# Performance work log

Hardware: AMD Instinct MI355X
Metric: run time of the kernel (lower is better)

Reference implementation:

```python
import jax, jax.numpy as jnp
import numpy as np
import math

D_MODEL = 768
H = 12
D_K = D_MODEL // H
KSIZE = 3  # 2*suppression_radius+1


def setup_inputs() -> dict:
    key = jax.random.key(0)
    ks = jax.random.split(key, 12)
    B, S = 8, 1024
    s = 1.0 / math.sqrt(D_MODEL)
    return {
        "q": jax.random.normal(ks[0], (B, S, D_MODEL), jnp.float32),
        "k": jax.random.normal(ks[1], (B, S, D_MODEL), jnp.float32),
        "v": jax.random.normal(ks[2], (B, S, D_MODEL), jnp.float32),
        "wq": jax.random.normal(ks[3], (D_MODEL, D_MODEL), jnp.float32) * s,
        "bq": jnp.zeros((D_MODEL,), jnp.float32),
        "wk": jax.random.normal(ks[4], (D_MODEL, D_MODEL), jnp.float32) * s,
        "bk": jnp.zeros((D_MODEL,), jnp.float32),
        "wv": jax.random.normal(ks[5], (D_MODEL, D_MODEL), jnp.float32) * s,
        "bv": jnp.zeros((D_MODEL,), jnp.float32),
        "wo": jax.random.normal(ks[6], (D_MODEL, D_MODEL), jnp.float32) * s,
        "bo": jnp.zeros((D_MODEL,), jnp.float32),
        "conv_w": jax.random.normal(ks[7], (H, 1, KSIZE, KSIZE), jnp.float32) * 0.1,
    }


def reference(q, k, v, wq, bq, wk, bk, wv, bv, wo, bo, conv_w):
    B, S, _ = q.shape
    # projections -> [B, h, S, d_k]
    Q = (q @ wq.T + bq).reshape(B, S, H, D_K).transpose(0, 2, 1, 3)
    K = (k @ wk.T + bk).reshape(B, S, H, D_K).transpose(0, 2, 1, 3)
    V = (v @ wv.T + bv).reshape(B, S, H, D_K).transpose(0, 2, 1, 3)
    scale = 1.0 / math.sqrt(D_K)
    scores = jnp.einsum("bhqd,bhkd->bhqk", Q, K) * scale  # [B,h,S,S]
    # per-head depthwise 3x3 conv over the score "image" (SAME padding, no bias)
    supp = jax.lax.conv_general_dilated(
        scores, conv_w, window_strides=(1, 1), padding="SAME",
        dimension_numbers=("NCHW", "OIHW", "NCHW"), feature_group_count=H)
    probs = jax.nn.softmax(scores - supp, axis=-1)
    out = jnp.einsum("bhqk,bhkd->bhqd", probs, V)
    out = out.transpose(0, 2, 1, 3).reshape(B, S, D_MODEL)
    return out @ wo.T + bo
```

## Files before the change

### kernel.cpp

```cpp
#include <hip/hip_runtime.h>
#include <math.h>

typedef __attribute__((ext_vector_type(8))) short short8;
typedef __attribute__((ext_vector_type(4))) float f32x4;
typedef __attribute__((ext_vector_type(16))) float f32x16;
typedef __attribute__((ext_vector_type(4))) unsigned short ushort4v;
typedef __attribute__((ext_vector_type(4))) unsigned int u32x4;

#define D_MODEL 768
#define NH      12
#define DK      64
#define SEQ     1024
#define NB      8
#define MTOT    (NB*SEQ)
#define NELT    ((size_t)MTOT*D_MODEL)
#define WELT    ((size_t)D_MODEL*D_MODEL)
#define L2E     1.44269504088896f

__device__ __forceinline__ unsigned short f2bf(float f) {
    unsigned int u = __builtin_bit_cast(unsigned int, f);
    unsigned int r = (u + 0x7FFFu + ((u >> 16) & 1u)) >> 16;
    return (unsigned short)r;
}
__device__ __forceinline__ float bf2f(unsigned short h) {
    return __builtin_bit_cast(float, ((unsigned int)h) << 16);
}
__device__ __forceinline__ float fast_exp2(float x) {
#if __has_builtin(__builtin_amdgcn_exp2f)
    return __builtin_amdgcn_exp2f(x);
#else
    return __expf(x * 0.69314718056f);
#endif
}
__device__ __forceinline__ unsigned int pk_bf16_rn(float lo, float hi) {
    unsigned int ul = __builtin_bit_cast(unsigned int, lo) + 0x8000u;
    unsigned int uh = __builtin_bit_cast(unsigned int, hi) + 0x8000u;
    return __builtin_amdgcn_perm(uh, ul, 0x07060302u);
}
__device__ __forceinline__ void plswap(unsigned int &a, unsigned int &b, int g) {
#if __has_builtin(__builtin_amdgcn_permlane32_swap)
    typedef __attribute__((ext_vector_type(2))) unsigned int uint2v;
    uint2v r = __builtin_amdgcn_permlane32_swap(a, b, false, false);
    a = r[0]; b = r[1];
#else
    unsigned int sa = __shfl_xor(a, 32), sb = __shfl_xor(b, 32);
    unsigned int na = g ? sb : a;
    unsigned int nb = g ? b : sa;
    a = na; b = nb;
#endif
}
__device__ __forceinline__ void gload_lds16(const void* g, void* lds) {
    __builtin_amdgcn_global_load_lds(
        (const __attribute__((address_space(1))) unsigned int*)g,
        (__attribute__((address_space(3))) unsigned int*)lds, 16, 0, 0);
}

__global__ __launch_bounds__(256) void cvt_all(
    const float* __restrict__ q, const float* __restrict__ k, const float* __restrict__ v,
    const float* __restrict__ wq, const float* __restrict__ wk,
    const float* __restrict__ wv, const float* __restrict__ wo,
    unsigned short* __restrict__ qb, unsigned short* __restrict__ kb, unsigned short* __restrict__ vb,
    unsigned short* __restrict__ wqb, unsigned short* __restrict__ wkb,
    unsigned short* __restrict__ wvb, unsigned short* __restrict__ wob)
{
    size_t i = (size_t)blockIdx.x * 256 + threadIdx.x;
    const size_t per = NELT / 8, wper = WELT / 8;
    const float* s; unsigned short* d; size_t l;
    if (i < per)            { s = q;  d = qb;  l = i; }
    else if (i < 2*per)     { s = k;  d = kb;  l = i - per; }
    else if (i < 3*per)     { s = v;  d = vb;  l = i - 2*per; }
    else {
        size_t j = i - 3*per;
        if (j < wper)        { s = wq; d = wqb; l = j; }
        else if (j < 2*wper) { s = wk; d = wkb; l = j - wper; }
        else if (j < 3*wper) { s = wv; d = wvb; l = j - 2*wper; }
        else                 { s = wo; d = wob; l = j - 3*wper; }
    }
    const float4* sp = (const float4*)(s + l*8);
    float4 v0 = sp[0], v1 = sp[1];
    short8 o;
    o[0]=(short)f2bf(v0.x); o[1]=(short)f2bf(v0.y); o[2]=(short)f2bf(v0.z); o[3]=(short)f2bf(v0.w);
    o[4]=(short)f2bf(v1.x); o[5]=(short)f2bf(v1.y); o[6]=(short)f2bf(v1.z); o[7]=(short)f2bf(v1.w);
    *(short8*)(d + l*8) = o;
}

#define BM 128
#define BN 128
#define BKG 64

__global__ __launch_bounds__(256) void proj_gemm(
    const unsigned short* __restrict__ Aq, const unsigned short* __restrict__ Ak,
    const unsigned short* __restrict__ Av,
    const unsigned short* __restrict__ Wq, const unsigned short* __restrict__ Wk,
    const unsigned short* __restrict__ Wv,
    const float* __restrict__ bq, const float* __restrict__ bk, const float* __restrict__ bv,
    unsigned short* __restrict__ Qp, unsigned short* __restrict__ Kp,
    unsigned short* __restrict__ Vtp)
{
    __shared__ unsigned short As[BM*BKG];
    __shared__ unsigned short Bs[BN*BKG];
    const int tid = threadIdx.x;
    const int lane = tid & 63, wid = tid >> 6;
    const int wr = wid >> 1, wc = wid & 1;
    const int m0 = blockIdx.y * BM, n0 = blockIdx.x * BN;
    const int z = blockIdx.z;

    const unsigned short* A = (z == 0) ? Aq : (z == 1) ? Ak : Av;
    const unsigned short* W = (z == 0) ? Wq : (z == 1) ? Wk : Wv;
    const float* bias       = (z == 0) ? bq : (z == 1) ? bk : bv;

    f32x4 acc[4][4];
    #pragma unroll
    for (int i = 0; i < 4; ++i)
        #pragma unroll
        for (int j = 0; j < 4; ++j) acc[i][j] = (f32x4)(0.f);

    for (int k0 = 0; k0 < D_MODEL; k0 += BKG) {
        __syncthreads();
        #pragma unroll
        for (int j = 0; j < 4; ++j) {
            int p = ((wid*4 + j) << 9) + lane*8;
            int row = p >> 6, off = p & 63;
            const unsigned short* srcA = A + (size_t)(m0+row)*D_MODEL + k0 + (off ^ ((row&7)<<3));
            gload_lds16(srcA, &As[(wid*4 + j) << 9]);
            const unsigned short* srcB = W + (size_t)(n0+row)*D_MODEL + k0 + (off ^ ((row&7)<<3));
            gload_lds16(srcB, &Bs[(wid*4 + j) << 9]);
        }
        __syncthreads();
        #pragma unroll
        for (int ks = 0; ks < 2; ++ks) {
            short8 af[4], bf8[4];
            #pragma unroll
            for (int mi = 0; mi < 4; ++mi) {
                int row = wr*64 + mi*16 + (lane & 15);
                af[mi] = *(const short8*)&As[row*BKG + ((ks*32 + (lane>>4)*8) ^ ((row&7)<<3))];
            }
            #pragma unroll
            for (int ni = 0; ni < 4; ++ni) {
                int row = wc*64 + ni*16 + (lane & 15);
                bf8[ni] = *(const short8*)&Bs[row*BKG + ((ks*32 + (lane>>4)*8) ^ ((row&7)<<3))];
            }
            #pragma unroll
            for (int mi = 0; mi < 4; ++mi)
                #pragma unroll
                for (int ni = 0; ni < 4; ++ni)
                    acc[mi][ni] = __builtin_amdgcn_mfma_f32_16x16x32_bf16(af[mi], bf8[ni], acc[mi][ni], 0, 0, 0);
        }
    }

    float bv4[4];
    #pragma unroll
    for (int ni = 0; ni < 4; ++ni) bv4[ni] = bias[n0 + wc*64 + ni*16 + (lane & 15)];

    if (z < 2) {
        unsigned short* C = (z == 0) ? Qp : Kp;
        const float scale = (z == 0) ? 0.125f : 1.0f;
        #pragma unroll
        for (int mi = 0; mi < 4; ++mi)
            #pragma unroll
            for (int ni = 0; ni < 4; ++ni) {
                int col = n0 + wc*64 + ni*16 + (lane & 15);
                int rbase = m0 + wr*64 + mi*16 + ((lane>>4)<<2);
                #pragma unroll
                for (int j = 0; j < 4; ++j)
                    C[(size_t)(rbase+j)*D_MODEL + col] = f2bf((acc[mi][ni][j] + bv4[ni]) * scale);
            }
    } else {
        #pragma unroll
        for (int mi = 0; mi < 4; ++mi)
            #pragma unroll
            for (int ni = 0; ni < 4; ++ni) {
                int col = n0 + wc*64 + ni*16 + (lane & 15);
                int hh = col >> 6, dd = col & 63;
                int m = m0 + wr*64 + mi*16 + ((lane>>4)<<2);
                int bb = m >> 10, ss = m & (SEQ-1);
                ushort4v pk;
                #pragma unroll
                for (int j = 0; j < 4; ++j) pk[j] = f2bf(acc[mi][ni][j] + bv4[ni]);
                *(ushort4v*)&Vtp[((size_t)(bb*NH + hh)*DK + dd)*SEQ + ss] = pk;
            }
    }
}

__global__ __launch_bounds__(256) void gemm_out(
    const unsigned short* __restrict__ A, const unsigned short* __restrict__ W,
    const float* __restrict__ bias, float* __restrict__ C)
{
    __shared__ unsigned short As[BM*BKG];
    __shared__ unsigned short Bs[BN*BKG];
    const int tid = threadIdx.x;
    const int lane = tid & 63, wid = tid >> 6;
    const int wr = wid >> 1, wc = wid & 1;
    const int m0 = blockIdx.y * BM, n0 = blockIdx.x * BN;

    f32x4 acc[4][4];
    #pragma unroll
    for (int i = 0; i < 4; ++i)
        #pragma unroll
        for (int j = 0; j < 4; ++j) acc[i][j] = (f32x4)(0.f);

    for (int k0 = 0; k0 < D_MODEL; k0 += BKG) {
        __syncthreads();
        #pragma unroll
        for (int j = 0; j < 4; ++j) {
            int p = ((wid*4 + j) << 9) + lane*8;
            int row = p >> 6, off = p & 63;
            const unsigned short* srcA = A + (size_t)(m0+row)*D_MODEL + k0 + (off ^ ((row&7)<<3));
            gload_lds16(srcA, &As[(wid*4 + j) << 9]);
            const unsigned short* srcB = W + (size_t)(n0+row)*D_MODEL + k0 + (off ^ ((row&7)<<3));
            gload_lds16(srcB, &Bs[(wid*4 + j) << 9]);
        }
        __syncthreads();
        #pragma unroll
        for (int ks = 0; ks < 2; ++ks) {
            short8 af[4], bf8[4];
            #pragma unroll
            for (int mi = 0; mi < 4; ++mi) {
                int row = wr*64 + mi*16 + (lane & 15);
                af[mi] = *(const short8*)&As[row*BKG + ((ks*32 + (lane>>4)*8) ^ ((row&7)<<3))];
            }
            #pragma unroll
            for (int ni = 0; ni < 4; ++ni) {
                int row = wc*64 + ni*16 + (lane & 15);
                bf8[ni] = *(const short8*)&Bs[row*BKG + ((ks*32 + (lane>>4)*8) ^ ((row&7)<<3))];
            }
            #pragma unroll
            for (int mi = 0; mi < 4; ++mi)
                #pragma unroll
                for (int ni = 0; ni < 4; ++ni)
                    acc[mi][ni] = __builtin_amdgcn_mfma_f32_16x16x32_bf16(af[mi], bf8[ni], acc[mi][ni], 0, 0, 0);
        }
    }

    float bv4[4];
    #pragma unroll
    for (int ni = 0; ni < 4; ++ni) bv4[ni] = bias[n0 + wc*64 + ni*16 + (lane & 15)];

    #pragma unroll
    for (int mi = 0; mi < 4; ++mi)
        #pragma unroll
        for (int ni = 0; ni < 4; ++ni) {
            int col = n0 + wc*64 + ni*16 + (lane & 15);
            int rbase = m0 + wr*64 + mi*16 + ((lane>>4)<<2);
            #pragma unroll
            for (int j = 0; j < 4; ++j)
                C[(size_t)(rbase+j)*D_MODEL + col] = acc[mi][ni][j] + bv4[ni];
        }
}

#define KVB 64
#define NCH (SEQ/KVB)
#define THR 8.0f

__global__ __launch_bounds__(256, 3) void attn_flash(
    const unsigned short* __restrict__ Qp,
    const unsigned short* __restrict__ Kp,
    const unsigned short* __restrict__ Vt,
    const float* __restrict__ CW,
    unsigned short* __restrict__ Aop)
{
    __shared__ unsigned short Ks[2][66*64];
    __shared__ unsigned short Vs[2][64*64];

    const int tid = threadIdx.x;
    const int lane = tid & 63, wid = tid >> 6;
    const int ql = lane & 31, g = lane >> 5;

    const int bid = blockIdx.x;
    const int sw = (bid & 7) * 96 + (bid >> 3);
    const int q0 = (sw & 7) * 128;
    const int bh = sw >> 3;
    const int h = bh % NH, b = bh / NH;

    float wcv[9];
    #pragma unroll
    for (int i = 0; i < 9; ++i) wcv[i] = CW[h*9 + i];

    const unsigned short* KpB = Kp + (size_t)b*SEQ*D_MODEL + h*DK;
    const unsigned short* QpB = Qp + (size_t)b*SEQ*D_MODEL + h*DK;
    const char* VtB = (const char*)Vt + (size_t)bh*DK*SEQ*2;

    short8 kreg[3];
    auto kload = [&](int ck) {
        #pragma unroll
        for (int u = 0; u < 3; ++u) {
            int idx = tid + u*256;
            short8 v = (short8)0;
            if (idx < 528) {
                int r = idx >> 3, oct = idx & 7;
                int gk = ck*KVB - 1 + r;
                if (gk >= 0 && gk < SEQ)
                    v = *(const short8*)&KpB[(size_t)gk*D_MODEL + oct*8];
            }
            kreg[u] = v;
        }
    };
    auto kstore = [&](int buf) {
        #pragma unroll
        for (int u = 0; u < 3; ++u) {
            int idx = tid + u*256;
            if (idx < 528) {
                int r = idx >> 3, oct = idx & 7;
                *(short8*)&Ks[buf][r*64 + ((oct ^ (r&7)) << 3)] = kreg[u];
            }
        }
    };
    auto vstage = [&](int ck, int buf) {
        #pragma unroll
        for (int u = 0; u < 2; ++u) {
            int p = (tid + u*256) * 16;
            int row = p >> 7, off = p & 127;
            const char* src = VtB + ((size_t)row*SEQ + ck*KVB)*2 + (off ^ ((row&7)<<4));
            gload_lds16(src, (char*)Vs[buf] + p);
        }
    };

    kload(0);

    short8 qtf[3][4];
    {
        int gq = q0 + wid*32 + ql;
        #pragma unroll
        for (int i = 0; i < 4; ++i) {
            int dwin = i*16 + g*8;
            short8 qm = (short8)0, qc, qp8 = (short8)0;
            if (gq > 0)      qm  = *(const short8*)&QpB[(size_t)(gq-1)*D_MODEL + dwin];
            qc = *(const short8*)&QpB[(size_t)gq*D_MODEL + dwin];
            if (gq < SEQ-1)  qp8 = *(const short8*)&QpB[(size_t)(gq+1)*D_MODEL + dwin];
            short8 f0, f1, f2;
            #pragma unroll
            for (int j = 0; j < 8; ++j) {
                float fm = bf2f((unsigned short)qm[j]);
                float fc = bf2f((unsigned short)qc[j]);
                float fp = bf2f((unsigned short)qp8[j]);
                float t0 = (fc - (wcv[1]*fm + wcv[4]*fc + wcv[7]*fp)) * L2E;
                float t1 = -(wcv[0]*fm + wcv[3]*fc + wcv[6]*fp) * L2E;
                float t2 = -(wcv[2]*fm + wcv[5]*fc + wcv[8]*fp) * L2E;
                f0[j] = (short)f2bf(t0);
                f1[j] = (short)f2bf(t1);
                f2[j] = (short)f2bf(t2);
            }
            qtf[0][i] = f0; qtf[1][i] = f1; qtf[2][i] = f2;
        }
    }
    kstore(0);
    vstage(0, 0);
    __syncthreads();

    float m = -1e30f, l = 0.f;
    f32x16 oac[2];
    oac[0] = (f32x16)(0.f); oac[1] = (f32x16)(0.f);

    int cur = 0;
    for (int ck = 0; ck < NCH; ++ck) {
        if (ck < NCH-1) { kload(ck+1); vstage(ck+1, cur^1); }

        f32x16 st2[2];
        #pragma unroll
        for (int t = 0; t < 2; ++t) {
            f32x16 s = (f32x16)(0.f);
            #pragma unroll
            for (int sl = 0; sl < 3; ++sl) {
                const int shift = (sl == 0) ? 1 : (sl == 1) ? 0 : 2;
                int ar = t*32 + ql + shift;
                #pragma unroll
                for (int i = 0; i < 4; ++i) {
                    int oct = 2*i + g;
                    short8 a = *(const short8*)&Ks[cur][ar*64 + ((oct ^ (ar&7)) << 3)];
                    s = __builtin_amdgcn_mfma_f32_32x32x16_bf16(a, qtf[sl][i], s, 0, 0, 0);
                }
            }
            st2[t] = s;
        }

        float tmax = -1e30f;
        #pragma unroll
        for (int t = 0; t < 2; ++t)
            #pragma unroll
            for (int j = 0; j < 16; ++j) tmax = fmaxf(tmax, st2[t][j]);
        tmax = fmaxf(tmax, __shfl_xor(tmax, 32));

        if (!__all(tmax - m <= THR)) {
            float mn = fmaxf(m, tmax);
            float r = fast_exp2(m - mn);
            l *= r;
            #pragma unroll
            for (int dt = 0; dt < 2; ++dt)
                #pragma unroll
                for (int j = 0; j < 16; ++j) oac[dt][j] *= r;
            m = mn;
        }
        float lsum = 0.f;
        #pragma unroll
        for (int t = 0; t < 2; ++t)
            #pragma unroll
            for (int j = 0; j < 16; ++j) {
                float e = fast_exp2(st2[t][j] - m);
                st2[t][j] = e;
                lsum += e;
            }
        lsum += __shfl_xor(lsum, 32);
        l += lsum;

        short8 pf[4];
        #pragma unroll
        for (int t = 0; t < 2; ++t) {
            #pragma unroll
            for (int f = 0; f < 2; ++f) {
                const int base = f*8;
                unsigned int x0 = pk_bf16_rn(st2[t][base+0], st2[t][base+1]);
                unsigned int x1 = pk_bf16_rn(st2[t][base+2], st2[t][base+3]);
                unsigned int y0 = pk_bf16_rn(st2[t][base+4], st2[t][base+5]);
                unsigned int y1 = pk_bf16_rn(st2[t][base+6], st2[t][base+7]);
                plswap(x0, y0, g);
                plswap(x1, y1, g);
                u32x4 w = {x0, x1, y0, y1};
                pf[t*2 + f] = __builtin_bit_cast(short8, w);
            }
        }

        #pragma unroll
        for (int f = 0; f < 4; ++f) {
            #pragma unroll
            for (int dt = 0; dt < 2; ++dt) {
                int vr = dt*32 + ql;
                int oct = 2*f + g;
                short8 a = *(const short8*)&Vs[cur][vr*64 + ((oct ^ (vr&7)) << 3)];
                oac[dt] = __builtin_amdgcn_mfma_f32_32x32x16_bf16(a, pf[f], oac[dt], 0, 0, 0);
            }
        }

        if (ck < NCH-1) kstore(cur^1);
        __syncthreads();
        cur ^= 1;
    }

    float invl = 1.0f / l;
    int qg = q0 + wid*32 + ql;
    size_t obase = (size_t)(b*SEQ + qg)*D_MODEL + h*DK;
    #pragma unroll
    for (int dt = 0; dt < 2; ++dt) {
        #pragma unroll
        for (int u = 0; u < 4; ++u) {
            int d0 = dt*32 + 8*u + 4*g;
            ushort4v o;
            #pragma unroll
            for (int j = 0; j < 4; ++j) o[j] = f2bf(oac[dt][4*u + j] * invl);
            *(ushort4v*)&Aop[obase + d0] = o;
        }
    }
}

extern "C" void kernel_launch(void* const* d_in, const int* in_sizes, int n_in,
                              void* d_out, int out_size, void* d_ws, size_t ws_size,
                              hipStream_t stream)
{
    const float* q  = (const float*)d_in[0];
    const float* k  = (const float*)d_in[1];
    const float* v  = (const float*)d_in[2];
    const float* wq = (const float*)d_in[3];
    const float* bq = (const float*)d_in[4];
    const float* wk = (const float*)d_in[5];
    const float* bk = (const float*)d_in[6];
    const float* wv = (const float*)d_in[7];
    const float* bv = (const float*)d_in[8];
    const float* wo = (const float*)d_in[9];
    const float* bo = (const float*)d_in[10];
    const float* cw = (const float*)d_in[11];

    unsigned short* qb  = (unsigned short*)d_ws;
    unsigned short* kb  = qb  + NELT;
    unsigned short* vb  = kb  + NELT;
    unsigned short* wqb = vb  + NELT;
    unsigned short* wkb = wqb + WELT;
    unsigned short* wvb = wkb + WELT;
    unsigned short* wob = wvb + WELT;
    unsigned short* Qp  = wob + WELT;
    unsigned short* Kp  = Qp  + NELT;
    unsigned short* Vtp = Kp  + NELT;
    unsigned short* Aop = Vtp + NELT;

    const int cvtBlocks = (int)((3*NELT + 4*WELT) / 8 / 256);
    cvt_all<<<cvtBlocks, 256, 0, stream>>>(q, k, v, wq, wk, wv, wo,
                                           qb, kb, vb, wqb, wkb, wvb, wob);

    dim3 gg(D_MODEL/BN, MTOT/BM, 3);
    proj_gemm<<<gg, 256, 0, stream>>>(qb, kb, vb, wqb, wkb, wvb, bq, bk, bv, Qp, Kp, Vtp);

    attn_flash<<<dim3(768), 256, 0, stream>>>(Qp, Kp, Vtp, cw, Aop);

    gemm_out<<<dim3(D_MODEL/BN, MTOT/BM), 256, 0, stream>>>(Aop, wob, bo, (float*)d_out);
}
```

Baseline: 165.1 us.

## Fuse activation fp32-to-bf16 conversion into projection GEMM and remap blocks per XCD

Drops the separate pass that converted the q/k/v activations to bf16. The projection GEMM now loads fp32 activation tiles straight into LDS with a swizzled layout and converts them to bf16 when building the MFMA fragments, so one full write and re-read of three bf16 activation tensors goes away. It also flattens the launch grid and maps block ids so each XCD covers a contiguous range of M tiles, aiming for better L2 reuse. In exchange, A tiles take twice the LDS and global-load bandwidth per tile, and every k-step repeats the conversion work across the column warps.

```diff
diff --git a/kernel.cpp b/kernel.cpp
--- a/kernel.cpp
+++ b/kernel.cpp
@@ -1,4 +1,5 @@
 #include <hip/hip_runtime.h>
+#include <hip/hip_bf16.h>
 #include <math.h>
 
 typedef __attribute__((ext_vector_type(8))) short short8;
@@ -21,6 +22,10 @@
     unsigned int u = __builtin_bit_cast(unsigned int, f);
     unsigned int r = (u + 0x7FFFu + ((u >> 16) & 1u)) >> 16;
     return (unsigned short)r;
+}
+__device__ __forceinline__ unsigned short f2bf_rne(float f) {
+    __hip_bfloat16 h = __float2bfloat16(f);
+    return __builtin_bit_cast(unsigned short, h);
 }
 __device__ __forceinline__ float bf2f(unsigned short h) {
     return __builtin_bit_cast(float, ((unsigned int)h) << 16);
@@ -55,27 +60,19 @@
         (__attribute__((address_space(3))) unsigned int*)lds, 16, 0, 0);
 }
 
-__global__ __launch_bounds__(256) void cvt_all(
-    const float* __restrict__ q, const float* __restrict__ k, const float* __restrict__ v,
-    const float* __restrict__ wq, const float* __restrict__ wk,
-    const float* __restrict__ wv, const float* __restrict__ wo,
-    unsigned short* __restrict__ qb, unsigned short* __restrict__ kb, unsigned short* __restrict__ vb,
-    unsigned short* __restrict__ wqb, unsigned short* __restrict__ wkb,
-    unsigned short* __restrict__ wvb, unsigned short* __restrict__ wob)
+__global__ __launch_bounds__(256) void cvt_w(
+    const float* __restrict__ a, const float* __restrict__ b,
+    const float* __restrict__ c, const float* __restrict__ e,
+    unsigned short* __restrict__ oa, unsigned short* __restrict__ ob,
+    unsigned short* __restrict__ oc, unsigned short* __restrict__ oe)
 {
     size_t i = (size_t)blockIdx.x * 256 + threadIdx.x;
-    const size_t per = NELT / 8, wper = WELT / 8;
+    const size_t per = WELT / 8;
     const float* s; unsigned short* d; size_t l;
-    if (i < per)            { s = q;  d = qb;  l = i; }
-    else if (i < 2*per)     { s = k;  d = kb;  l = i - per; }
-    else if (i < 3*per)     { s = v;  d = vb;  l = i - 2*per; }
-    else {
-        size_t j = i - 3*per;
-        if (j < wper)        { s = wq; d = wqb; l = j; }
-        else if (j < 2*wper) { s = wk; d = wkb; l = j - wper; }
-        else if (j < 3*wper) { s = wv; d = wvb; l = j - 2*wper; }
-        else                 { s = wo; d = wob; l = j - 3*wper; }
-    }
+    if (i < per)        { s = a; d = oa; l = i; }
+    else if (i < 2*per) { s = b; d = ob; l = i - per; }
+    else if (i < 3*per) { s = c; d = oc; l = i - 2*per; }
+    else                { s = e; d = oe; l = i - 3*per; }
     const float4* sp = (const float4*)(s + l*8);
     float4 v0 = sp[0], v1 = sp[1];
     short8 o;
@@ -89,23 +86,28 @@
 #define BKG 64
 
 __global__ __launch_bounds__(256) void proj_gemm(
-    const unsigned short* __restrict__ Aq, const unsigned short* __restrict__ Ak,
-    const unsigned short* __restrict__ Av,
+    const float* __restrict__ Aq, const float* __restrict__ Ak, const float* __restrict__ Av,
     const unsigned short* __restrict__ Wq, const unsigned short* __restrict__ Wk,
     const unsigned short* __restrict__ Wv,
     const float* __restrict__ bq, const float* __restrict__ bk, const float* __restrict__ bv,
     unsigned short* __restrict__ Qp, unsigned short* __restrict__ Kp,
     unsigned short* __restrict__ Vtp)
 {
-    __shared__ unsigned short As[BM*BKG];
+    __shared__ float Asf[BM*BKG];
     __shared__ unsigned short Bs[BN*BKG];
     const int tid = threadIdx.x;
     const int lane = tid & 63, wid = tid >> 6;
     const int wr = wid >> 1, wc = wid & 1;
-    const int m0 = blockIdx.y * BM, n0 = blockIdx.x * BN;
-    const int z = blockIdx.z;
-
-    const unsigned short* A = (z == 0) ? Aq : (z == 1) ? Ak : Av;
+
+    const int bid = blockIdx.x;
+    const int xcd = bid & 7;
+    const int j = bid >> 3;
+    const int mzL = j / 6, n = j % 6;
+    const int mz = xcd * 24 + mzL;
+    const int z = mz >> 6;
+    const int m0 = (mz & 63) * BM, n0 = n * BN;
+
+    const float* A          = (z == 0) ? Aq : (z == 1) ? Ak : Av;
     const unsigned short* W = (z == 0) ? Wq : (z == 1) ? Wk : Wv;
     const float* bias       = (z == 0) ? bq : (z == 1) ? bk : bv;
 
@@ -113,18 +115,23 @@
     #pragma unroll
     for (int i = 0; i < 4; ++i)
         #pragma unroll
-        for (int j = 0; j < 4; ++j) acc[i][j] = (f32x4)(0.f);
+        for (int jj = 0; jj < 4; ++jj) acc[i][jj] = (f32x4)(0.f);
 
     for (int k0 = 0; k0 < D_MODEL; k0 += BKG) {
         __syncthreads();
         #pragma unroll
-        for (int j = 0; j < 4; ++j) {
-            int p = ((wid*4 + j) << 9) + lane*8;
+        for (int c = 0; c < 8; ++c) {
+            int gI = ((wid*8 + c) << 6) + lane;
+            int row = gI >> 4, gran = gI & 15;
+            const float* srcA = A + (size_t)(m0+row)*D_MODEL + k0 + ((gran ^ (row & 15)) << 2);
+            gload_lds16(srcA, (char*)Asf + ((wid*8 + c) << 10));
+        }
+        #pragma unroll
+        for (int c = 0; c < 4; ++c) {
+            int p = ((wid*4 + c) << 9) + lane*8;
             int row = p >> 6, off = p & 63;
-            const unsigned short* srcA = A + (size_t)(m0+row)*D_MODEL + k0 + (off ^ ((row&7)<<3));
-            gload_lds16(srcA, &As[(wid*4 + j) << 9]);
             const unsigned short* srcB = W + (size_t)(n0+row)*D_MODEL + k0 + (off ^ ((row&7)<<3));
-            gload_lds16(srcB, &Bs[(wid*4 + j) << 9]);
+            gload_lds16(srcB, &Bs[(wid*4 + c) << 9]);
         }
         __syncthreads();
         #pragma unroll
@@ -133,7 +140,17 @@
             #pragma unroll
             for (int mi = 0; mi < 4; ++mi) {
                 int row = wr*64 + mi*16 + (lane & 15);
-                af[mi] = *(const short8*)&As[row*BKG + ((ks*32 + (lane>>4)*8) ^ ((row&7)<<3))];
+                int g0 = ks*8 + ((lane >> 4) << 1);
+                const float* r0 = Asf + row*64 + ((g0 ^ (row & 15)) << 2);
+                const float* r1 = Asf + row*64 + (((g0+1) ^ (row & 15)) << 2);
+                float4 a0 = *(const float4*)r0;
+                float4 a1 = *(const float4*)r1;
+                short8 v;
+                v[0]=(short)f2bf_rne(a0.x); v[1]=(short)f2bf_rne(a0.y);
+                v[2]=(short)f2bf_rne(a0.z); v[3]=(short)f2bf_rne(a0.w);
+                v[4]=(short)f2bf_rne(a1.x); v[5]=(short)f2bf_rne(a1.y);
+                v[6]=(short)f2bf_rne(a1.z); v[7]=(short)f2bf_rne(a1.w);
+                af[mi] = v;
             }
             #pragma unroll
             for (int ni = 0; ni < 4; ++ni) {
@@ -162,8 +179,8 @@
                 int col = n0 + wc*64 + ni*16 + (lane & 15);
                 int rbase = m0 + wr*64 + mi*16 + ((lane>>4)<<2);
                 #pragma unroll
-                for (int j = 0; j < 4; ++j)
-                    C[(size_t)(rbase+j)*D_MODEL + col] = f2bf((acc[mi][ni][j] + bv4[ni]) * scale);
+                for (int jj = 0; jj < 4; ++jj)
+                    C[(size_t)(rbase+jj)*D_MODEL + col] = f2bf((acc[mi][ni][jj] + bv4[ni]) * scale);
             }
     } else {
         #pragma unroll
@@ -172,11 +189,11 @@
             for (int ni = 0; ni < 4; ++ni) {
                 int col = n0 + wc*64 + ni*16 + (lane & 15);
                 int hh = col >> 6, dd = col & 63;
-                int m = m0 + wr*64 + mi*16 + ((lane>>4)<<2);
-                int bb = m >> 10, ss = m & (SEQ-1);
+                int mrow = m0 + wr*64 + mi*16 + ((lane>>4)<<2);
+                int bb = mrow >> 10, ss = mrow & (SEQ-1);
                 ushort4v pk;
                 #pragma unroll
-                for (int j = 0; j < 4; ++j) pk[j] = f2bf(acc[mi][ni][j] + bv4[ni]);
+                for (int jj = 0; jj < 4; ++jj) pk[jj] = f2bf(acc[mi][ni][jj] + bv4[ni]);
                 *(ushort4v*)&Vtp[((size_t)(bb*NH + hh)*DK + dd)*SEQ + ss] = pk;
             }
     }
@@ -468,10 +485,7 @@
     const float* bo = (const float*)d_in[10];
     const float* cw = (const float*)d_in[11];
 
-    unsigned short* qb  = (unsigned short*)d_ws;
-    unsigned short* kb  = qb  + NELT;
-    unsigned short* vb  = kb  + NELT;
-    unsigned short* wqb = vb  + NELT;
+    unsigned short* wqb = (unsigned short*)d_ws;
     unsigned short* wkb = wqb + WELT;
     unsigned short* wvb = wkb + WELT;
     unsigned short* wob = wvb + WELT;
@@ -480,12 +494,10 @@
     unsigned short* Vtp = Kp  + NELT;
     unsigned short* Aop = Vtp + NELT;
 
-    const int cvtBlocks = (int)((3*NELT + 4*WELT) / 8 / 256);
-    cvt_all<<<cvtBlocks, 256, 0, stream>>>(q, k, v, wq, wk, wv, wo,
-                                           qb, kb, vb, wqb, wkb, wvb, wob);
-
-    dim3 gg(D_MODEL/BN, MTOT/BM, 3);
-    proj_gemm<<<gg, 256, 0, stream>>>(qb, kb, vb, wqb, wkb, wvb, bq, bk, bv, Qp, Kp, Vtp);
+    cvt_w<<<(int)(4*WELT/8/256), 256, 0, stream>>>(wq, wk, wv, wo, wqb, wkb, wvb, wob);
+
+    proj_gemm<<<dim3(1152), 256, 0, stream>>>(q, k, v, wqb, wkb, wvb,
+                                              bq, bk, bv, Qp, Kp, Vtp);
 
     attn_flash<<<dim3(768), 256, 0, stream>>>(Qp, Kp, Vtp, cw, Aop);
 
```

Result: faster. 155.1 us (-6.1%).
